# Performance work log

Measured on AMD Instinct MI355X. Metric: run time of the kernel, lower is better.

The kernel has to match this reference:

```python
import jax, jax.numpy as jnp
import numpy as np

NEG_SLOPE = 0.2
H = 2  # num_heads (hardcoded in the torch module)


def _gat_conv(x, W, al, ar, b, src, dst, n_nodes):
    """DGL GATConv: x [N,F] -> [N,H,D]."""
    D = al.shape[1]
    h = (x @ W).reshape(n_nodes, H, D)               # [N,H,D]
    el = jnp.einsum('nhd,hd->nh', h, al)              # [N,H]
    er = jnp.einsum('nhd,hd->nh', h, ar)              # [N,H]
    e = el[src] + er[dst]                             # [E,H]
    e = jnp.where(e >= 0, e, NEG_SLOPE * e)           # LeakyReLU
    # edge softmax over incoming edges of each dst (every node has a self loop)
    m = jax.ops.segment_max(e, dst, num_segments=n_nodes)      # [N,H]
    ex = jnp.exp(e - m[dst])                                    # [E,H]
    s = jax.ops.segment_sum(ex, dst, num_segments=n_nodes)     # [N,H]
    alpha = ex / s[dst]                                         # [E,H]
    msg = alpha[:, :, None] * h[src]                             # [E,H,D]
    out = jax.ops.segment_sum(msg, dst, num_segments=n_nodes)   # [N,H,D]
    return out + b.reshape(1, H, D)


def setup_inputs() -> dict:
    key = jax.random.key(0)
    ks = jax.random.split(key, 10)
    N, E, F_IN, HID, OUT = 100000, 1600000, 128, 64, 64
    sc = 0.05
    return {
        'x':   jax.random.normal(ks[0], (N, F_IN), jnp.float32),
        'src': jax.random.randint(ks[1], (E,), 0, N, jnp.int32),
        'dst': jax.random.randint(ks[2], (E,), 0, N, jnp.int32),
        'W1':  jax.random.normal(ks[3], (F_IN, H * HID), jnp.float32) * sc,
        'al1': jax.random.normal(ks[4], (H, HID), jnp.float32) * sc,
        'ar1': jax.random.normal(ks[5], (H, HID), jnp.float32) * sc,
        'b1':  jnp.zeros((H * HID,), jnp.float32),
        'W2':  jax.random.normal(ks[6], (H * HID, H * OUT), jnp.float32) * sc,
        'al2': jax.random.normal(ks[7], (H, OUT), jnp.float32) * sc,
        'ar2': jax.random.normal(ks[8], (H, OUT), jnp.float32) * sc,
        'b2':  jnp.zeros((H * OUT,), jnp.float32),
    }


def reference(x, src, dst, W1, al1, ar1, b1, W2, al2, ar2, b2):
    N = x.shape[0]
    # dgl.add_self_loop
    loop = jnp.arange(N, dtype=src.dtype)
    s = jnp.concatenate([src, loop])
    d = jnp.concatenate([dst, loop])
    h = _gat_conv(x, W1, al1, ar1, b1, s, d, N)       # [N,H,HID]
    h = jax.nn.relu(h).reshape(N, -1)                  # flatten heads
    out = _gat_conv(h, W2, al2, ar2, b2, s, d, N)      # [N,H,OUT]
    return out.reshape(N, -1)
```

## Files before the change

kernel.cpp:

```cpp
#include <hip/hip_runtime.h>
#include <hip/hip_fp16.h>


#define NEG_SLOPE 0.2f
#define BSHIFT 8
#define ETILE 4096

typedef _Float16 half8_t __attribute__((ext_vector_type(8)));
typedef float f32x4_t __attribute__((ext_vector_type(4)));


__global__ __launch_bounds__(256) void k_bcount(const int* __restrict__ dst, int E,
                                                int nbuck, int* __restrict__ bcnt) {
    __shared__ int cnt[512];
    int t = threadIdx.x;
    for (int b = t; b < nbuck; b += 256) cnt[b] = 0;
    __syncthreads();
    int e0 = blockIdx.x * ETILE;
    #pragma unroll
    for (int j = 0; j < ETILE / 256; j++) {
        int e = e0 + j * 256 + t;
        if (e < E) atomicAdd(&cnt[dst[e] >> BSHIFT], 1);
    }
    __syncthreads();
    for (int b = t; b < nbuck; b += 256) {
        int c = cnt[b];
        if (c > 0) atomicAdd(&bcnt[b], c);
    }
}

__global__ __launch_bounds__(256) void k_bscan(const int* __restrict__ bcnt, int nbuck,
                                               int* __restrict__ bbase,
                                               int* __restrict__ bcursor,
                                               int* __restrict__ rowStart, int N, int E) {
    __shared__ int sa[512], sb[512];
    int t = threadIdx.x;
    sa[t] = (t < nbuck) ? bcnt[t] : 0;
    sa[t + 256] = (t + 256 < nbuck) ? bcnt[t + 256] : 0;
    __syncthreads();
    int* a = sa;
    int* b = sb;
    for (int off = 1; off < 512; off <<= 1) {
        b[t] = a[t] + ((t >= off) ? a[t - off] : 0);
        int i = t + 256;
        b[i] = a[i] + ((i >= off) ? a[i - off] : 0);
        __syncthreads();
        int* tmp = a; a = b; b = tmp;
    }
    #pragma unroll
    for (int k = 0; k < 2; k++) {
        int i = t + k * 256;
        if (i <= nbuck) {
            int e_ = (i == 0) ? 0 : a[i - 1];
            bbase[i] = e_;
            if (i < nbuck) bcursor[i] = e_;
        }
    }
    if (t == 0) rowStart[N] = E;
}

__global__ __launch_bounds__(256) void k_bucket(const int* __restrict__ src,
                                                const int* __restrict__ dst, int E,
                                                int nbuck, int* __restrict__ bcursor,
                                                int* __restrict__ ebuf) {
    __shared__ int cnt[512];
    __shared__ int base[512];
    int t = threadIdx.x;
    for (int b = t; b < nbuck; b += 256) cnt[b] = 0;
    __syncthreads();
    int e0 = blockIdx.x * ETILE;
    int dv[ETILE / 256], sv[ETILE / 256];
    #pragma unroll
    for (int j = 0; j < ETILE / 256; j++) {
        int e = e0 + j * 256 + t;
        dv[j] = -1;
        if (e < E) {
            dv[j] = dst[e];
            sv[j] = src[e];
            atomicAdd(&cnt[dv[j] >> BSHIFT], 1);
        }
    }
    __syncthreads();
    for (int b = t; b < nbuck; b += 256) {
        int c = cnt[b];
        base[b] = (c > 0) ? atomicAdd(&bcursor[b], c) : 0;
    }
    __syncthreads();
    for (int b = t; b < nbuck; b += 256) cnt[b] = 0;
    __syncthreads();
    #pragma unroll
    for (int j = 0; j < ETILE / 256; j++) {
        if (dv[j] >= 0) {
            int bk = dv[j] >> BSHIFT;
            int r = atomicAdd(&cnt[bk], 1);
            ebuf[base[bk] + r] = sv[j] | ((dv[j] & ((1 << BSHIFT) - 1)) << 17);
        }
    }
}

__global__ __launch_bounds__(256) void k_build(const int* __restrict__ ebuf,
                                               const int* __restrict__ bbase,
                                               int* __restrict__ rowStart,
                                               int* __restrict__ csr, int N) {
    __shared__ int dcnt[256];
    __shared__ int sa[256], sb[256];
    __shared__ int cur[256];
    int b = blockIdx.x;
    int t = threadIdx.x;
    int lo = bbase[b], hi = bbase[b + 1];
    int n0 = b << BSHIFT;
    dcnt[t] = 0;
    __syncthreads();
    for (int p = lo + t; p < hi; p += 256)
        atomicAdd(&dcnt[((unsigned)ebuf[p]) >> 17], 1);
    __syncthreads();
    sa[t] = dcnt[t];
    __syncthreads();
    int* a = sa;
    int* bq = sb;
    for (int off = 1; off < 256; off <<= 1) {
        bq[t] = a[t] + ((t >= off) ? a[t - off] : 0);
        __syncthreads();
        int* tmp = a; a = bq; bq = tmp;
    }
    int excl = (t == 0) ? 0 : a[t - 1];
    int pos0 = lo + excl;
    if (n0 + t < N) rowStart[n0 + t] = pos0;
    cur[t] = pos0;
    __syncthreads();
    for (int p = lo + t; p < hi; p += 256) {
        int v = ebuf[p];
        int pos = atomicAdd(&cur[((unsigned)v) >> 17], 1);
        csr[pos] = v & 0x1FFFF;
    }
}


__global__ __launch_bounds__(256) void k_prep(const float* __restrict__ W1,
                                              const float* __restrict__ W2,
                                              __half* __restrict__ wh1,
                                              __half* __restrict__ wh2,
                                              int* __restrict__ bcnt, int nbuck) {
    int b = blockIdx.x;
    if (b >= 16) {
        for (int i = threadIdx.x; i < nbuck; i += 256) bcnt[i] = 0;
        return;
    }
    const float* W = (b < 8) ? W1 : W2;
    __half* Wh = (b < 8) ? wh1 : wh2;
    int q = (b & 7) * 256 + threadIdx.x;
    int r = q >> 4;
    int c = q & 15;
    int cl = c ^ (r & 7);
    float f[8];
    #pragma unroll
    for (int j = 0; j < 8; j++) f[j] = W[(size_t)(cl * 8 + j) * 128 + r];
    __half2 h0 = __floats2half2_rn(f[0], f[1]);
    __half2 h1 = __floats2half2_rn(f[2], f[3]);
    __half2 h2 = __floats2half2_rn(f[4], f[5]);
    __half2 h3 = __floats2half2_rn(f[6], f[7]);
    uint4 pk;
    pk.x = *(unsigned*)&h0;
    pk.y = *(unsigned*)&h1;
    pk.z = *(unsigned*)&h2;
    pk.w = *(unsigned*)&h3;
    *(uint4*)((char*)Wh + (size_t)q * 16) = pk;
}


__device__ __forceinline__ void g2l16(const void* g, void* l) {
    __builtin_amdgcn_global_load_lds((const __attribute__((address_space(1))) void*)g,
                                     (__attribute__((address_space(3))) void*)l, 16, 0, 0);
}

template <bool FP16IN>
__global__ __launch_bounds__(256, 3) void k_gemm_fused(const void* __restrict__ Ain,
                                                       const __half* __restrict__ WhT,
                                                       __half* __restrict__ hb,
                                                       const float* __restrict__ al,
                                                       const float* __restrict__ ar,
                                                       float* __restrict__ el,
                                                       float* __restrict__ er, int M) {
    __shared__ __half xs[64 * 128];
    __shared__ __half ws[128 * 128];
    int row0 = blockIdx.x * 64;
    int t = threadIdx.x;

    for (int j = 0; j < 8; j++) {
        int c16 = t + j * 256;
        g2l16((const char*)WhT + (size_t)c16 * 16, (char*)ws + (size_t)c16 * 16);
    }
    if (FP16IN) {
        const char* Ah = (const char*)Ain;
        for (int j = 0; j < 4; j++) {
            int c16 = t + j * 256;
            g2l16(Ah + (size_t)row0 * 256 + (size_t)c16 * 16, (char*)xs + (size_t)c16 * 16);
        }
    } else {
        const float* A = (const float*)Ain;
        for (int j = 0; j < 8; j++) {
            int f4 = t + j * 256;
            int r = f4 >> 5;
            int gr = row0 + r;
            if (gr >= M) gr = M - 1;
            float4 v = ((const float4*)(A + (size_t)gr * 128))[f4 & 31];
            __half2 h0 = __floats2half2_rn(v.x, v.y);
            __half2 h1 = __floats2half2_rn(v.z, v.w);
            uint2 pk;
            pk.x = *(unsigned*)&h0;
            pk.y = *(unsigned*)&h1;
            int h8 = f4 & 31;
            int c = h8 >> 1, hh = h8 & 1;
            int addr8 = r * 32 + (c ^ (r & 7)) * 2 + hh;
            *(uint2*)((char*)xs + (size_t)addr8 * 8) = pk;
        }
    }
    __syncthreads();

    int wid = t >> 6, lane = t & 63;
    int l15 = lane & 15;
    int g = lane >> 4;
    int mrow = wid * 16 + l15;

    half8_t xf[4];
    #pragma unroll
    for (int ks = 0; ks < 4; ks++) {
        int c = ks * 4 + g;
        xf[ks] = *(const half8_t*)((const char*)xs + mrow * 256 + (size_t)(c ^ (mrow & 7)) * 16);
    }

    f32x4_t acc[8];
    #pragma unroll
    for (int i = 0; i < 8; i++) acc[i] = (f32x4_t){0.f, 0.f, 0.f, 0.f};

    #pragma unroll
    for (int nt = 0; nt < 8; nt++) {
        int nrow = nt * 16 + l15;
        #pragma unroll
        for (int ks = 0; ks < 4; ks++) {
            int c = ks * 4 + g;
            half8_t wf = *(const half8_t*)((const char*)ws + nrow * 256 + (size_t)(c ^ (nrow & 7)) * 16);
            acc[nt] = __builtin_amdgcn_mfma_f32_16x16x32_f16(wf, xf[ks], acc[nt], 0, 0, 0);
        }
    }

    int m = row0 + wid * 16 + l15;
    bool valid = m < M;
    float plh0 = 0.f, prh0 = 0.f, plh1 = 0.f, prh1 = 0.f;
    #pragma unroll
    for (int nt = 0; nt < 8; nt++) {
        int col0 = nt * 16 + g * 4;
        if (valid) {
            __half2 p0 = __floats2half2_rn(acc[nt][0], acc[nt][1]);
            __half2 p1 = __floats2half2_rn(acc[nt][2], acc[nt][3]);
            uint2 pk;
            pk.x = *(unsigned*)&p0;
            pk.y = *(unsigned*)&p1;
            *(uint2*)(hb + (size_t)m * 128 + col0) = pk;
        }
        float4 alv = *(const float4*)(al + col0);
        float4 arv = *(const float4*)(ar + col0);
        float pl = acc[nt][0] * alv.x + acc[nt][1] * alv.y + acc[nt][2] * alv.z + acc[nt][3] * alv.w;
        float pr = acc[nt][0] * arv.x + acc[nt][1] * arv.y + acc[nt][2] * arv.z + acc[nt][3] * arv.w;
        if (nt < 4) { plh0 += pl; prh0 += pr; }
        else       { plh1 += pl; prh1 += pr; }
    }
    plh0 += __shfl_xor(plh0, 16); plh0 += __shfl_xor(plh0, 32);
    plh1 += __shfl_xor(plh1, 16); plh1 += __shfl_xor(plh1, 32);
    prh0 += __shfl_xor(prh0, 16); prh0 += __shfl_xor(prh0, 32);
    prh1 += __shfl_xor(prh1, 16); prh1 += __shfl_xor(prh1, 32);
    if (lane < 16 && valid) {
        el[m * 2 + 0] = plh0;
        el[m * 2 + 1] = plh1;
        er[m * 2 + 0] = prh0;
        er[m * 2 + 1] = prh1;
    }
}


__device__ __forceinline__ float h2f(__half h) { return __half2float(h); }

template <bool RELU, bool FP16OUT>
__global__ __launch_bounds__(256) void k_agg(const __half* __restrict__ hb,
                                             const float* __restrict__ el,
                                             const float* __restrict__ er,
                                             const int* __restrict__ rowStart,
                                             const int* __restrict__ csr,
                                             const float* __restrict__ bias,
                                             void* __restrict__ outv, int N) {
    __shared__ uint2 albuf[4][64];
    int wave = threadIdx.x >> 6;
    int lane = threadIdx.x & 63;
    int n = blockIdx.x * 4 + wave;
    if (n >= N) return;

    int rs = rowStart[n];
    int deg = rowStart[n + 1] - rs;
    float2 erv = ((const float2*)er)[n];

    if (deg < 64) {
        int sreg = n;
        float e0 = -3e38f, e1 = -3e38f;
        if (lane <= deg) {
            sreg = (lane == deg) ? n : csr[rs + lane];
            float2 ev = ((const float2*)el)[sreg];
            e0 = ev.x + erv.x;
            e0 = (e0 >= 0.f) ? e0 : NEG_SLOPE * e0;
            e1 = ev.y + erv.y;
            e1 = (e1 >= 0.f) ? e1 : NEG_SLOPE * e1;
        }
        float ex0 = __expf(e0);
        float ex1 = __expf(e1);
        float s0 = ex0, s1 = ex1;
        for (int off = 32; off > 0; off >>= 1) {
            s0 += __shfl_xor(s0, off);
            s1 += __shfl_xor(s1, off);
        }
        __half2 ah = __floats2half2_rn(ex0 * (1.0f / s0), ex1 * (1.0f / s1));
        uint2 pk;
        pk.x = (unsigned)sreg;
        pk.y = *(unsigned*)&ah;
        albuf[wave][lane] = pk;

        int q = lane >> 4;
        int c = lane & 15;
        float acc0 = 0.f, acc1 = 0.f, acc2 = 0.f, acc3 = 0.f;
        float acc4 = 0.f, acc5 = 0.f, acc6 = 0.f, acc7 = 0.f;
        int iters = (deg + 4) >> 2;
        #pragma unroll 4
        for (int kk = 0; kk < iters; ++kk) {
            int j = 4 * kk + q;
            uint2 pj = albuf[wave][j];
            __half2 ahj = *(__half2*)&pj.y;
            float a = (c >= 8) ? h2f(ahj.y) : h2f(ahj.x);
            uint4 hv = ((const uint4*)(hb + (size_t)pj.x * 128))[c];
            __half2 h0 = *(__half2*)&hv.x;
            __half2 h1 = *(__half2*)&hv.y;
            __half2 h2 = *(__half2*)&hv.z;
            __half2 h3 = *(__half2*)&hv.w;
            acc0 += a * h2f(h0.x);  acc1 += a * h2f(h0.y);
            acc2 += a * h2f(h1.x);  acc3 += a * h2f(h1.y);
            acc4 += a * h2f(h2.x);  acc5 += a * h2f(h2.y);
            acc6 += a * h2f(h3.x);  acc7 += a * h2f(h3.y);
        }
        acc0 += __shfl_xor(acc0, 16); acc1 += __shfl_xor(acc1, 16);
        acc2 += __shfl_xor(acc2, 16); acc3 += __shfl_xor(acc3, 16);
        acc4 += __shfl_xor(acc4, 16); acc5 += __shfl_xor(acc5, 16);
        acc6 += __shfl_xor(acc6, 16); acc7 += __shfl_xor(acc7, 16);
        acc0 += __shfl_xor(acc0, 32); acc1 += __shfl_xor(acc1, 32);
        acc2 += __shfl_xor(acc2, 32); acc3 += __shfl_xor(acc3, 32);
        acc4 += __shfl_xor(acc4, 32); acc5 += __shfl_xor(acc5, 32);
        acc6 += __shfl_xor(acc6, 32); acc7 += __shfl_xor(acc7, 32);
        if (lane < 16) {
            const float4* bp = (const float4*)(bias + c * 8);
            float4 b0 = bp[0], b1 = bp[1];
            float o0 = acc0 + b0.x, o1 = acc1 + b0.y, o2 = acc2 + b0.z, o3 = acc3 + b0.w;
            float o4 = acc4 + b1.x, o5 = acc5 + b1.y, o6 = acc6 + b1.z, o7 = acc7 + b1.w;
            if (RELU) {
                o0 = fmaxf(o0, 0.f); o1 = fmaxf(o1, 0.f); o2 = fmaxf(o2, 0.f); o3 = fmaxf(o3, 0.f);
                o4 = fmaxf(o4, 0.f); o5 = fmaxf(o5, 0.f); o6 = fmaxf(o6, 0.f); o7 = fmaxf(o7, 0.f);
            }
            if (FP16OUT) {
                __half2 q0 = __floats2half2_rn(o0, o1);
                __half2 q1 = __floats2half2_rn(o2, o3);
                __half2 q2 = __floats2half2_rn(o4, o5);
                __half2 q3 = __floats2half2_rn(o6, o7);
                uint4 opk;
                opk.x = *(unsigned*)&q0;
                opk.y = *(unsigned*)&q1;
                opk.z = *(unsigned*)&q2;
                opk.w = *(unsigned*)&q3;
                ((uint4*)((__half*)outv + (size_t)n * 128))[c ^ (n & 7)] = opk;
            } else {
                float* op = (float*)outv + (size_t)n * 128 + c * 8;
                ((float4*)op)[0] = make_float4(o0, o1, o2, o3);
                ((float4*)op)[1] = make_float4(o4, o5, o6, o7);
            }
        }
    } else {
        float m0 = -3e38f, m1 = -3e38f;
        for (int i = lane; i <= deg; i += 64) {
            int s = (i == deg) ? n : csr[rs + i];
            float2 ev = ((const float2*)el)[s];
            float e0 = ev.x + erv.x;
            e0 = (e0 >= 0.f) ? e0 : NEG_SLOPE * e0;
            float e1 = ev.y + erv.y;
            e1 = (e1 >= 0.f) ? e1 : NEG_SLOPE * e1;
            m0 = fmaxf(m0, e0);
            m1 = fmaxf(m1, e1);
        }
        for (int off = 32; off > 0; off >>= 1) {
            m0 = fmaxf(m0, __shfl_xor(m0, off));
            m1 = fmaxf(m1, __shfl_xor(m1, off));
        }
        float s0 = 0.f, s1 = 0.f;
        for (int i = lane; i <= deg; i += 64) {
            int s = (i == deg) ? n : csr[rs + i];
            float2 ev = ((const float2*)el)[s];
            float e0 = ev.x + erv.x;
            e0 = (e0 >= 0.f) ? e0 : NEG_SLOPE * e0;
            float e1 = ev.y + erv.y;
            e1 = (e1 >= 0.f) ? e1 : NEG_SLOPE * e1;
            s0 += __expf(e0 - m0);
            s1 += __expf(e1 - m1);
        }
        for (int off = 32; off > 0; off >>= 1) {
            s0 += __shfl_xor(s0, off);
            s1 += __shfl_xor(s1, off);
        }
        float inv0 = 1.0f / s0, inv1 = 1.0f / s1;
        float mh = (lane < 32) ? m0 : m1;
        float invh = (lane < 32) ? inv0 : inv1;
        float erh = (lane < 32) ? erv.x : erv.y;
        float a0 = 0.f, a1 = 0.f;
        for (int j = 0; j <= deg; j++) {
            int sj = (j == deg) ? n : csr[rs + j];
            float elh = el[sj * 2 + (lane >> 5)];
            float e = elh + erh;
            e = (e >= 0.f) ? e : NEG_SLOPE * e;
            float alpha = __expf(e - mh) * invh;
            unsigned hv = ((const unsigned*)(hb + (size_t)sj * 128))[lane];
            __half2 h = *(__half2*)&hv;
            a0 += alpha * h2f(h.x);
            a1 += alpha * h2f(h.y);
        }
        float2 bv = ((const float2*)bias)[lane];
        a0 += bv.x;
        a1 += bv.y;
        if (RELU) {
            a0 = fmaxf(a0, 0.f);
            a1 = fmaxf(a1, 0.f);
        }
        if (FP16OUT) {
            __half2 hv2 = __floats2half2_rn(a0, a1);
            int chunk = lane >> 2;
            int sub = lane & 3;
            *(unsigned*)((char*)outv + (size_t)n * 256 +
                         (size_t)((chunk ^ (n & 7)) * 16 + sub * 4)) = *(unsigned*)&hv2;
        } else {
            ((float2*)((float*)outv + (size_t)n * 128))[lane] = make_float2(a0, a1);
        }
    }
}


static inline size_t align_up(size_t v, size_t a) { return (v + a - 1) & ~(a - 1); }

extern "C" void kernel_launch(void* const* d_in, const int* in_sizes, int n_in,
                              void* d_out, int out_size, void* d_ws, size_t ws_size,
                              hipStream_t stream) {
    const float* x   = (const float*)d_in[0];
    const int*   src = (const int*)d_in[1];
    const int*   dst = (const int*)d_in[2];
    const float* W1  = (const float*)d_in[3];
    const float* al1 = (const float*)d_in[4];
    const float* ar1 = (const float*)d_in[5];
    const float* b1  = (const float*)d_in[6];
    const float* W2  = (const float*)d_in[7];
    const float* al2 = (const float*)d_in[8];
    const float* ar2 = (const float*)d_in[9];
    const float* b2  = (const float*)d_in[10];
    float* out = (float*)d_out;

    const int N = in_sizes[0] / 128;
    const int E = in_sizes[1];
    const int NBUCK = (N + 255) >> 8;

    char* ws = (char*)d_ws;
    size_t off = 0;
    __half* bufBh = (__half*)(ws + off); off = align_up(off + (size_t)N * 128 * 2, 256);
    __half* hb    = (__half*)(ws + off); off = align_up(off + (size_t)N * 128 * 2, 256);
    float* el   = (float*)(ws + off); off = align_up(off + (size_t)N * 2 * 4, 256);
    float* er   = (float*)(ws + off); off = align_up(off + (size_t)N * 2 * 4, 256);
    int* rowStart = (int*)(ws + off); off = align_up(off + (size_t)(N + 1) * 4, 256);
    int* csr      = (int*)(ws + off); off = align_up(off + (size_t)E * 4, 256);
    int* ebuf     = (int*)(ws + off); off = align_up(off + (size_t)E * 4, 256);
    int* bcnt     = (int*)(ws + off); off = align_up(off + (size_t)NBUCK * 4, 256);
    int* bbase    = (int*)(ws + off); off = align_up(off + (size_t)(NBUCK + 1) * 4, 256);
    int* bcursor  = (int*)(ws + off); off = align_up(off + (size_t)NBUCK * 4, 256);
    __half* wh1   = (__half*)(ws + off); off = align_up(off + (size_t)16384 * 2, 256);
    __half* wh2   = (__half*)(ws + off); off = align_up(off + (size_t)16384 * 2, 256);

    const int etile_grid = (E + ETILE - 1) / ETILE;

    k_prep<<<17, 256, 0, stream>>>(W1, W2, wh1, wh2, bcnt, NBUCK);
    k_bcount<<<etile_grid, 256, 0, stream>>>(dst, E, NBUCK, bcnt);
    k_bscan<<<1, 256, 0, stream>>>(bcnt, NBUCK, bbase, bcursor, rowStart, N, E);
    k_bucket<<<etile_grid, 256, 0, stream>>>(src, dst, E, NBUCK, bcursor, ebuf);
    k_build<<<NBUCK, 256, 0, stream>>>(ebuf, bbase, rowStart, csr, N);

    const int gemm_grid = (N + 63) / 64;
    const int agg_grid = (N + 3) / 4;

    k_gemm_fused<false><<<gemm_grid, 256, 0, stream>>>(x, wh1, hb, al1, ar1, el, er, N);
    k_agg<true, true><<<agg_grid, 256, 0, stream>>>(hb, el, er, rowStart, csr, b1, bufBh, N);

    k_gemm_fused<true><<<gemm_grid, 256, 0, stream>>>(bufBh, wh2, hb, al2, ar2, el, er, N);
    k_agg<false, false><<<agg_grid, 256, 0, stream>>>(hb, el, er, rowStart, csr, b2, out, N);
}
```

Before: 236.6 us.

## Split aggregation into alpha pass and column-sliced gather over sliced feature layout

The GEMM now writes node features in eight 16-column slices, each a contiguous 32-byte-per-node array. A new k_alpha kernel computes the per-edge softmax weights and stores packed (src, alpha) records. A new k_aggs kernel gathers one slice per block so each slice's working set fits in cache. The intent is better L2 locality for the random gather, at the cost of an extra kernel, an extra E-sized record buffer write and read, and eight passes over the edge records.

Measured after the change: 628.8 us. 2.66x slower.

```diff
diff --git a/kernel.cpp b/kernel.cpp
--- a/kernel.cpp
+++ b/kernel.cpp
@@ -5,9 +5,11 @@
 #define NEG_SLOPE 0.2f
 #define BSHIFT 8
 #define ETILE 4096
+#define NPW 8
 
 typedef _Float16 half8_t __attribute__((ext_vector_type(8)));
 typedef float f32x4_t __attribute__((ext_vector_type(4)));
+typedef unsigned long long u64;
 
 
 __global__ __launch_bounds__(256) void k_bcount(const int* __restrict__ dst, int E,
@@ -176,7 +178,7 @@
 template <bool FP16IN>
 __global__ __launch_bounds__(256, 3) void k_gemm_fused(const void* __restrict__ Ain,
                                                        const __half* __restrict__ WhT,
-                                                       __half* __restrict__ hb,
+                                                       __half* __restrict__ hbs,
                                                        const float* __restrict__ al,
                                                        const float* __restrict__ ar,
                                                        float* __restrict__ el,
@@ -253,10 +255,9 @@
         if (valid) {
             __half2 p0 = __floats2half2_rn(acc[nt][0], acc[nt][1]);
             __half2 p1 = __floats2half2_rn(acc[nt][2], acc[nt][3]);
-            uint2 pk;
-            pk.x = *(unsigned*)&p0;
-            pk.y = *(unsigned*)&p1;
-            *(uint2*)(hb + (size_t)m * 128 + col0) = pk;
+            u64 w = ((u64)(*(unsigned*)&p1) << 32) | (u64)(*(unsigned*)&p0);
+            __builtin_nontemporal_store(
+                w, (u64*)((char*)hbs + ((size_t)nt * M + m) * 32 + (size_t)g * 8));
         }
         float4 alv = *(const float4*)(al + col0);
         float4 arv = *(const float4*)(ar + col0);
@@ -280,30 +281,26 @@
 
 __device__ __forceinline__ float h2f(__half h) { return __half2float(h); }
 
-template <bool RELU, bool FP16OUT>
-__global__ __launch_bounds__(256) void k_agg(const __half* __restrict__ hb,
-                                             const float* __restrict__ el,
-                                             const float* __restrict__ er,
-                                             const int* __restrict__ rowStart,
-                                             const int* __restrict__ csr,
-                                             const float* __restrict__ bias,
-                                             void* __restrict__ outv, int N) {
-    __shared__ uint2 albuf[4][64];
+__global__ __launch_bounds__(256) void k_alpha(const float* __restrict__ el,
+                                               const float* __restrict__ er,
+                                               const int* __restrict__ rowStart,
+                                               const int* __restrict__ csr,
+                                               u64* __restrict__ ea, int N) {
     int wave = threadIdx.x >> 6;
     int lane = threadIdx.x & 63;
     int n = blockIdx.x * 4 + wave;
     if (n >= N) return;
-
     int rs = rowStart[n];
     int deg = rowStart[n + 1] - rs;
     float2 erv = ((const float2*)er)[n];
+    size_t base = (size_t)rs + n;
 
     if (deg < 64) {
-        int sreg = n;
+        int sj = n;
         float e0 = -3e38f, e1 = -3e38f;
         if (lane <= deg) {
-            sreg = (lane == deg) ? n : csr[rs + lane];
-            float2 ev = ((const float2*)el)[sreg];
+            sj = (lane == deg) ? n : csr[rs + lane];
+            float2 ev = ((const float2*)el)[sj];
             e0 = ev.x + erv.x;
             e0 = (e0 >= 0.f) ? e0 : NEG_SLOPE * e0;
             e1 = ev.y + erv.y;
@@ -316,66 +313,10 @@
             s0 += __shfl_xor(s0, off);
             s1 += __shfl_xor(s1, off);
         }
-        __half2 ah = __floats2half2_rn(ex0 * (1.0f / s0), ex1 * (1.0f / s1));
-        uint2 pk;
-        pk.x = (unsigned)sreg;
-        pk.y = *(unsigned*)&ah;
-        albuf[wave][lane] = pk;
-
-        int q = lane >> 4;
-        int c = lane & 15;
-        float acc0 = 0.f, acc1 = 0.f, acc2 = 0.f, acc3 = 0.f;
-        float acc4 = 0.f, acc5 = 0.f, acc6 = 0.f, acc7 = 0.f;
-        int iters = (deg + 4) >> 2;
-        #pragma unroll 4
-        for (int kk = 0; kk < iters; ++kk) {
-            int j = 4 * kk + q;
-            uint2 pj = albuf[wave][j];
-            __half2 ahj = *(__half2*)&pj.y;
-            float a = (c >= 8) ? h2f(ahj.y) : h2f(ahj.x);
-            uint4 hv = ((const uint4*)(hb + (size_t)pj.x * 128))[c];
-            __half2 h0 = *(__half2*)&hv.x;
-            __half2 h1 = *(__half2*)&hv.y;
-            __half2 h2 = *(__half2*)&hv.z;
-            __half2 h3 = *(__half2*)&hv.w;
-            acc0 += a * h2f(h0.x);  acc1 += a * h2f(h0.y);
-            acc2 += a * h2f(h1.x);  acc3 += a * h2f(h1.y);
-            acc4 += a * h2f(h2.x);  acc5 += a * h2f(h2.y);
-            acc6 += a * h2f(h3.x);  acc7 += a * h2f(h3.y);
-        }
-        acc0 += __shfl_xor(acc0, 16); acc1 += __shfl_xor(acc1, 16);
-        acc2 += __shfl_xor(acc2, 16); acc3 += __shfl_xor(acc3, 16);
-        acc4 += __shfl_xor(acc4, 16); acc5 += __shfl_xor(acc5, 16);
-        acc6 += __shfl_xor(acc6, 16); acc7 += __shfl_xor(acc7, 16);
-        acc0 += __shfl_xor(acc0, 32); acc1 += __shfl_xor(acc1, 32);
-        acc2 += __shfl_xor(acc2, 32); acc3 += __shfl_xor(acc3, 32);
-        acc4 += __shfl_xor(acc4, 32); acc5 += __shfl_xor(acc5, 32);
-        acc6 += __shfl_xor(acc6, 32); acc7 += __shfl_xor(acc7, 32);
-        if (lane < 16) {
-            const float4* bp = (const float4*)(bias + c * 8);
-            float4 b0 = bp[0], b1 = bp[1];
-            float o0 = acc0 + b0.x, o1 = acc1 + b0.y, o2 = acc2 + b0.z, o3 = acc3 + b0.w;
-            float o4 = acc4 + b1.x, o5 = acc5 + b1.y, o6 = acc6 + b1.z, o7 = acc7 + b1.w;
-            if (RELU) {
-                o0 = fmaxf(o0, 0.f); o1 = fmaxf(o1, 0.f); o2 = fmaxf(o2, 0.f); o3 = fmaxf(o3, 0.f);
-                o4 = fmaxf(o4, 0.f); o5 = fmaxf(o5, 0.f); o6 = fmaxf(o6, 0.f); o7 = fmaxf(o7, 0.f);
-            }
-            if (FP16OUT) {
-                __half2 q0 = __floats2half2_rn(o0, o1);
-                __half2 q1 = __floats2half2_rn(o2, o3);
-                __half2 q2 = __floats2half2_rn(o4, o5);
-                __half2 q3 = __floats2half2_rn(o6, o7);
-                uint4 opk;
-                opk.x = *(unsigned*)&q0;
-                opk.y = *(unsigned*)&q1;
-                opk.z = *(unsigned*)&q2;
-                opk.w = *(unsigned*)&q3;
-                ((uint4*)((__half*)outv + (size_t)n * 128))[c ^ (n & 7)] = opk;
-            } else {
-                float* op = (float*)outv + (size_t)n * 128 + c * 8;
-                ((float4*)op)[0] = make_float4(o0, o1, o2, o3);
-                ((float4*)op)[1] = make_float4(o4, o5, o6, o7);
-            }
+        if (lane <= deg) {
+            __half2 ah = __floats2half2_rn(ex0 * (1.0f / s0), ex1 * (1.0f / s1));
+            u64 rec = ((u64)(*(unsigned*)&ah) << 32) | (u64)(unsigned)sj;
+            __builtin_nontemporal_store(rec, ea + base + lane);
         }
     } else {
         float m0 = -3e38f, m1 = -3e38f;
@@ -409,36 +350,89 @@
             s1 += __shfl_xor(s1, off);
         }
         float inv0 = 1.0f / s0, inv1 = 1.0f / s1;
-        float mh = (lane < 32) ? m0 : m1;
-        float invh = (lane < 32) ? inv0 : inv1;
-        float erh = (lane < 32) ? erv.x : erv.y;
-        float a0 = 0.f, a1 = 0.f;
-        for (int j = 0; j <= deg; j++) {
-            int sj = (j == deg) ? n : csr[rs + j];
-            float elh = el[sj * 2 + (lane >> 5)];
-            float e = elh + erh;
-            e = (e >= 0.f) ? e : NEG_SLOPE * e;
-            float alpha = __expf(e - mh) * invh;
-            unsigned hv = ((const unsigned*)(hb + (size_t)sj * 128))[lane];
-            __half2 h = *(__half2*)&hv;
-            a0 += alpha * h2f(h.x);
-            a1 += alpha * h2f(h.y);
-        }
-        float2 bv = ((const float2*)bias)[lane];
-        a0 += bv.x;
-        a1 += bv.y;
-        if (RELU) {
-            a0 = fmaxf(a0, 0.f);
-            a1 = fmaxf(a1, 0.f);
-        }
-        if (FP16OUT) {
-            __half2 hv2 = __floats2half2_rn(a0, a1);
-            int chunk = lane >> 2;
-            int sub = lane & 3;
-            *(unsigned*)((char*)outv + (size_t)n * 256 +
-                         (size_t)((chunk ^ (n & 7)) * 16 + sub * 4)) = *(unsigned*)&hv2;
-        } else {
-            ((float2*)((float*)outv + (size_t)n * 128))[lane] = make_float2(a0, a1);
+        for (int i = lane; i <= deg; i += 64) {
+            int s = (i == deg) ? n : csr[rs + i];
+            float2 ev = ((const float2*)el)[s];
+            float e0 = ev.x + erv.x;
+            e0 = (e0 >= 0.f) ? e0 : NEG_SLOPE * e0;
+            float e1 = ev.y + erv.y;
+            e1 = (e1 >= 0.f) ? e1 : NEG_SLOPE * e1;
+            __half2 ah = __floats2half2_rn(__expf(e0 - m0) * inv0, __expf(e1 - m1) * inv1);
+            u64 rec = ((u64)(*(unsigned*)&ah) << 32) | (u64)(unsigned)s;
+            __builtin_nontemporal_store(rec, ea + base + i);
+        }
+    }
+}
+
+
+template <bool RELU, bool FP16OUT>
+__global__ __launch_bounds__(256) void k_aggs(const u64* __restrict__ ea,
+                                              const __half* __restrict__ hbs,
+                                              const int* __restrict__ rowStart,
+                                              const float* __restrict__ bias,
+                                              void* __restrict__ outv, int N) {
+    int s = blockIdx.x & 7;
+    int ng = blockIdx.x >> 3;
+    int wid = threadIdx.x >> 6;
+    int lane = threadIdx.x & 63;
+    int g = lane >> 2;
+    int d = lane & 3;
+    const char* slice = (const char*)hbs + (size_t)s * N * 32;
+    float4 bv = *(const float4*)(bias + s * 16 + d * 4);
+    bool head1 = (s >= 4);
+    int n0 = (ng * 4 + wid) * NPW;
+
+    for (int ni = 0; ni < NPW; ni++) {
+        int n = n0 + ni;
+        if (n >= N) return;
+        int rs = rowStart[n];
+        int cnt = rowStart[n + 1] - rs + 1;
+        size_t base = (size_t)rs + n;
+        float a0 = 0.f, a1 = 0.f, a2 = 0.f, a3 = 0.f;
+        for (int j0 = 0; j0 < cnt; j0 += 16) {
+            int j = j0 + g;
+            if (j < cnt) {
+                u64 rec = __builtin_nontemporal_load(ea + base + j);
+                unsigned srcn = (unsigned)rec;
+                unsigned ab = (unsigned)(rec >> 32);
+                unsigned short hbits = (unsigned short)(head1 ? (ab >> 16) : (ab & 0xffff));
+                __half ha;
+                *(unsigned short*)&ha = hbits;
+                float a = h2f(ha);
+                uint2 hv = *(const uint2*)(slice + (size_t)srcn * 32 + (size_t)d * 8);
+                __half2 p0 = *(__half2*)&hv.x;
+                __half2 p1 = *(__half2*)&hv.y;
+                a0 += a * h2f(p0.x);
+                a1 += a * h2f(p0.y);
+                a2 += a * h2f(p1.x);
+                a3 += a * h2f(p1.y);
+            }
+        }
+        #pragma unroll
+        for (int off = 4; off < 64; off <<= 1) {
+            a0 += __shfl_xor(a0, off);
+            a1 += __shfl_xor(a1, off);
+            a2 += __shfl_xor(a2, off);
+            a3 += __shfl_xor(a3, off);
+        }
+        if (g == 0) {
+            a0 += bv.x; a1 += bv.y; a2 += bv.z; a3 += bv.w;
+            if (RELU) {
+                a0 = fmaxf(a0, 0.f); a1 = fmaxf(a1, 0.f);
+                a2 = fmaxf(a2, 0.f); a3 = fmaxf(a3, 0.f);
+            }
+            if (FP16OUT) {
+                __half2 q0 = __floats2half2_rn(a0, a1);
+                __half2 q1 = __floats2half2_rn(a2, a3);
+                u64 w = ((u64)(*(unsigned*)&q1) << 32) | (u64)(*(unsigned*)&q0);
+                int c = 2 * s + (d >> 1);
+                size_t addr = (size_t)n * 256 + (size_t)((c ^ (n & 7)) * 16 + (d & 1) * 8);
+                __builtin_nontemporal_store(w, (u64*)((char*)outv + addr));
+            } else {
+                f32x4_t o = {a0, a1, a2, a3};
+                __builtin_nontemporal_store(
+                    o, (f32x4_t*)((float*)outv + (size_t)n * 128 + s * 16 + d * 4));
+            }
         }
     }
 }
@@ -469,12 +463,13 @@
     char* ws = (char*)d_ws;
     size_t off = 0;
     __half* bufBh = (__half*)(ws + off); off = align_up(off + (size_t)N * 128 * 2, 256);
-    __half* hb    = (__half*)(ws + off); off = align_up(off + (size_t)N * 128 * 2, 256);
+    __half* hbs   = (__half*)(ws + off); off = align_up(off + (size_t)N * 128 * 2, 256);
     float* el   = (float*)(ws + off); off = align_up(off + (size_t)N * 2 * 4, 256);
     float* er   = (float*)(ws + off); off = align_up(off + (size_t)N * 2 * 4, 256);
     int* rowStart = (int*)(ws + off); off = align_up(off + (size_t)(N + 1) * 4, 256);
     int* csr      = (int*)(ws + off); off = align_up(off + (size_t)E * 4, 256);
     int* ebuf     = (int*)(ws + off); off = align_up(off + (size_t)E * 4, 256);
+    u64* ea       = (u64*)(ws + off); off = align_up(off + (size_t)(E + N) * 8, 256);
     int* bcnt     = (int*)(ws + off); off = align_up(off + (size_t)NBUCK * 4, 256);
     int* bbase    = (int*)(ws + off); off = align_up(off + (size_t)(NBUCK + 1) * 4, 256);
     int* bcursor  = (int*)(ws + off); off = align_up(off + (size_t)NBUCK * 4, 256);
@@ -490,11 +485,14 @@
     k_build<<<NBUCK, 256, 0, stream>>>(ebuf, bbase, rowStart, csr, N);
 
     const int gemm_grid = (N + 63) / 64;
-    const int agg_grid = (N + 3) / 4;
-
-    k_gemm_fused<false><<<gemm_grid, 256, 0, stream>>>(x, wh1, hb, al1, ar1, el, er, N);
-    k_agg<true, true><<<agg_grid, 256, 0, stream>>>(hb, el, er, rowStart, csr, b1, bufBh, N);
-
-    k_gemm_fused<true><<<gemm_grid, 256, 0, stream>>>(bufBh, wh2, hb, al2, ar2, el, er, N);
-    k_agg<false, false><<<agg_grid, 256, 0, stream>>>(hb, el, er, rowStart, csr, b2, out, N);
-}
+    const int alpha_grid = (N + 3) / 4;
+    const int aggs_grid = 8 * ((N + 4 * NPW - 1) / (4 * NPW));
+
+    k_gemm_fused<false><<<gemm_grid, 256, 0, stream>>>(x, wh1, hbs, al1, ar1, el, er, N);
+    k_alpha<<<alpha_grid, 256, 0, stream>>>(el, er, rowStart, csr, ea, N);
+    k_aggs<true, true><<<aggs_grid, 256, 0, stream>>>(ea, hbs, rowStart, b1, bufBh, N);
+
+    k_gemm_fused<true><<<gemm_grid, 256, 0, stream>>>(bufBh, wh2, hbs, al2, ar2, el, er, N);
+    k_alpha<<<alpha_grid, 256, 0, stream>>>(el, er, rowStart, csr, ea, N);
+    k_aggs<false, false><<<aggs_grid, 256, 0, stream>>>(ea, hbs, rowStart, b2, out, N);
+}
```

## Pack four nodes per wave in aggregation and fuse bucket count into GEMM

Applied to the files above, without the earlier changes.

The aggregation kernel now assigns a 16-lane quarter-wave to each destination node instead of a full wave. It computes unnormalized exponentials in one pass without a max subtraction and applies the softmax normalization once at the end. This is meant to remove wasted lanes on low-degree nodes and the separate max pass. The dst bucket-count kernel is folded into the first GEMM launch as extra blocks, saving one launch. Dropping the max subtraction risks overflow if attention logits grow large.

Measured after the change: 228.2 us. 3.6% less time.

```diff
diff --git a/kernel.cpp b/kernel.cpp
--- a/kernel.cpp
+++ b/kernel.cpp
@@ -8,26 +8,8 @@
 
 typedef _Float16 half8_t __attribute__((ext_vector_type(8)));
 typedef float f32x4_t __attribute__((ext_vector_type(4)));
-
-
-__global__ __launch_bounds__(256) void k_bcount(const int* __restrict__ dst, int E,
-                                                int nbuck, int* __restrict__ bcnt) {
-    __shared__ int cnt[512];
-    int t = threadIdx.x;
-    for (int b = t; b < nbuck; b += 256) cnt[b] = 0;
-    __syncthreads();
-    int e0 = blockIdx.x * ETILE;
-    #pragma unroll
-    for (int j = 0; j < ETILE / 256; j++) {
-        int e = e0 + j * 256 + t;
-        if (e < E) atomicAdd(&cnt[dst[e] >> BSHIFT], 1);
-    }
-    __syncthreads();
-    for (int b = t; b < nbuck; b += 256) {
-        int c = cnt[b];
-        if (c > 0) atomicAdd(&bcnt[b], c);
-    }
-}
+typedef unsigned long long u64;
+
 
 __global__ __launch_bounds__(256) void k_bscan(const int* __restrict__ bcnt, int nbuck,
                                                int* __restrict__ bbase,
@@ -173,19 +155,40 @@
                                      (__attribute__((address_space(3))) void*)l, 16, 0, 0);
 }
 
-template <bool FP16IN>
+template <bool FP16IN, bool COUNT>
 __global__ __launch_bounds__(256, 3) void k_gemm_fused(const void* __restrict__ Ain,
                                                        const __half* __restrict__ WhT,
                                                        __half* __restrict__ hb,
                                                        const float* __restrict__ al,
                                                        const float* __restrict__ ar,
                                                        float* __restrict__ el,
-                                                       float* __restrict__ er, int M) {
+                                                       float* __restrict__ er, int M,
+                                                       const int* __restrict__ dstE, int E,
+                                                       int nbuck, int* __restrict__ bcnt,
+                                                       int gemmBlocks) {
     __shared__ __half xs[64 * 128];
     __shared__ __half ws[128 * 128];
+    int t = threadIdx.x;
+
+    if (COUNT && (int)blockIdx.x >= gemmBlocks) {
+        int* cnt = (int*)xs;
+        for (int b = t; b < nbuck; b += 256) cnt[b] = 0;
+        __syncthreads();
+        int e0 = ((int)blockIdx.x - gemmBlocks) * ETILE;
+        #pragma unroll
+        for (int j = 0; j < ETILE / 256; j++) {
+            int e = e0 + j * 256 + t;
+            if (e < E) atomicAdd(&cnt[dstE[e] >> BSHIFT], 1);
+        }
+        __syncthreads();
+        for (int b = t; b < nbuck; b += 256) {
+            int c = cnt[b];
+            if (c > 0) atomicAdd(&bcnt[b], c);
+        }
+        return;
+    }
+
     int row0 = blockIdx.x * 64;
-    int t = threadIdx.x;
-
     for (int j = 0; j < 8; j++) {
         int c16 = t + j * 256;
         g2l16((const char*)WhT + (size_t)c16 * 16, (char*)ws + (size_t)c16 * 16);
@@ -288,157 +291,114 @@
                                              const int* __restrict__ csr,
                                              const float* __restrict__ bias,
                                              void* __restrict__ outv, int N) {
-    __shared__ uint2 albuf[4][64];
-    int wave = threadIdx.x >> 6;
+    __shared__ u64 albuf[4][4][65];
+    int wid = threadIdx.x >> 6;
     int lane = threadIdx.x & 63;
-    int n = blockIdx.x * 4 + wave;
-    if (n >= N) return;
-
-    int rs = rowStart[n];
-    int deg = rowStart[n + 1] - rs;
-    float2 erv = ((const float2*)er)[n];
-
-    if (deg < 64) {
-        int sreg = n;
-        float e0 = -3e38f, e1 = -3e38f;
-        if (lane <= deg) {
-            sreg = (lane == deg) ? n : csr[rs + lane];
-            float2 ev = ((const float2*)el)[sreg];
-            e0 = ev.x + erv.x;
-            e0 = (e0 >= 0.f) ? e0 : NEG_SLOPE * e0;
-            e1 = ev.y + erv.y;
-            e1 = (e1 >= 0.f) ? e1 : NEG_SLOPE * e1;
-        }
-        float ex0 = __expf(e0);
-        float ex1 = __expf(e1);
-        float s0 = ex0, s1 = ex1;
-        for (int off = 32; off > 0; off >>= 1) {
-            s0 += __shfl_xor(s0, off);
-            s1 += __shfl_xor(s1, off);
-        }
-        __half2 ah = __floats2half2_rn(ex0 * (1.0f / s0), ex1 * (1.0f / s1));
-        uint2 pk;
-        pk.x = (unsigned)sreg;
-        pk.y = *(unsigned*)&ah;
-        albuf[wave][lane] = pk;
-
-        int q = lane >> 4;
-        int c = lane & 15;
-        float acc0 = 0.f, acc1 = 0.f, acc2 = 0.f, acc3 = 0.f;
-        float acc4 = 0.f, acc5 = 0.f, acc6 = 0.f, acc7 = 0.f;
-        int iters = (deg + 4) >> 2;
-        #pragma unroll 4
-        for (int kk = 0; kk < iters; ++kk) {
-            int j = 4 * kk + q;
-            uint2 pj = albuf[wave][j];
-            __half2 ahj = *(__half2*)&pj.y;
-            float a = (c >= 8) ? h2f(ahj.y) : h2f(ahj.x);
-            uint4 hv = ((const uint4*)(hb + (size_t)pj.x * 128))[c];
-            __half2 h0 = *(__half2*)&hv.x;
-            __half2 h1 = *(__half2*)&hv.y;
-            __half2 h2 = *(__half2*)&hv.z;
-            __half2 h3 = *(__half2*)&hv.w;
-            acc0 += a * h2f(h0.x);  acc1 += a * h2f(h0.y);
-            acc2 += a * h2f(h1.x);  acc3 += a * h2f(h1.y);
-            acc4 += a * h2f(h2.x);  acc5 += a * h2f(h2.y);
-            acc6 += a * h2f(h3.x);  acc7 += a * h2f(h3.y);
-        }
-        acc0 += __shfl_xor(acc0, 16); acc1 += __shfl_xor(acc1, 16);
-        acc2 += __shfl_xor(acc2, 16); acc3 += __shfl_xor(acc3, 16);
-        acc4 += __shfl_xor(acc4, 16); acc5 += __shfl_xor(acc5, 16);
-        acc6 += __shfl_xor(acc6, 16); acc7 += __shfl_xor(acc7, 16);
-        acc0 += __shfl_xor(acc0, 32); acc1 += __shfl_xor(acc1, 32);
-        acc2 += __shfl_xor(acc2, 32); acc3 += __shfl_xor(acc3, 32);
-        acc4 += __shfl_xor(acc4, 32); acc5 += __shfl_xor(acc5, 32);
-        acc6 += __shfl_xor(acc6, 32); acc7 += __shfl_xor(acc7, 32);
-        if (lane < 16) {
-            const float4* bp = (const float4*)(bias + c * 8);
-            float4 b0 = bp[0], b1 = bp[1];
-            float o0 = acc0 + b0.x, o1 = acc1 + b0.y, o2 = acc2 + b0.z, o3 = acc3 + b0.w;
-            float o4 = acc4 + b1.x, o5 = acc5 + b1.y, o6 = acc6 + b1.z, o7 = acc7 + b1.w;
-            if (RELU) {
-                o0 = fmaxf(o0, 0.f); o1 = fmaxf(o1, 0.f); o2 = fmaxf(o2, 0.f); o3 = fmaxf(o3, 0.f);
-                o4 = fmaxf(o4, 0.f); o5 = fmaxf(o5, 0.f); o6 = fmaxf(o6, 0.f); o7 = fmaxf(o7, 0.f);
-            }
-            if (FP16OUT) {
-                __half2 q0 = __floats2half2_rn(o0, o1);
-                __half2 q1 = __floats2half2_rn(o2, o3);
-                __half2 q2 = __floats2half2_rn(o4, o5);
-                __half2 q3 = __floats2half2_rn(o6, o7);
-                uint4 opk;
-                opk.x = *(unsigned*)&q0;
-                opk.y = *(unsigned*)&q1;
-                opk.z = *(unsigned*)&q2;
-                opk.w = *(unsigned*)&q3;
-                ((uint4*)((__half*)outv + (size_t)n * 128))[c ^ (n & 7)] = opk;
-            } else {
-                float* op = (float*)outv + (size_t)n * 128 + c * 8;
-                ((float4*)op)[0] = make_float4(o0, o1, o2, o3);
-                ((float4*)op)[1] = make_float4(o4, o5, o6, o7);
-            }
-        }
-    } else {
-        float m0 = -3e38f, m1 = -3e38f;
-        for (int i = lane; i <= deg; i += 64) {
+    int q = lane >> 4;
+    int l = lane & 15;
+    int n = (blockIdx.x * 4 + wid) * 4 + q;
+    bool active = n < N;
+
+    int rs = 0, deg = 0;
+    float2 erv = make_float2(0.f, 0.f);
+    if (active) {
+        rs = rowStart[n];
+        deg = rowStart[n + 1] - rs;
+        erv = ((const float2*)er)[n];
+    }
+
+    float s0 = 0.f, s1 = 0.f;
+    if (active) {
+        for (int i = l; i <= deg; i += 16) {
             int s = (i == deg) ? n : csr[rs + i];
             float2 ev = ((const float2*)el)[s];
             float e0 = ev.x + erv.x;
             e0 = (e0 >= 0.f) ? e0 : NEG_SLOPE * e0;
             float e1 = ev.y + erv.y;
             e1 = (e1 >= 0.f) ? e1 : NEG_SLOPE * e1;
-            m0 = fmaxf(m0, e0);
-            m1 = fmaxf(m1, e1);
-        }
-        for (int off = 32; off > 0; off >>= 1) {
-            m0 = fmaxf(m0, __shfl_xor(m0, off));
-            m1 = fmaxf(m1, __shfl_xor(m1, off));
-        }
-        float s0 = 0.f, s1 = 0.f;
-        for (int i = lane; i <= deg; i += 64) {
-            int s = (i == deg) ? n : csr[rs + i];
+            float ex0 = __expf(e0);
+            float ex1 = __expf(e1);
+            s0 += ex0;
+            s1 += ex1;
+            if (i < 64) {
+                __half2 eh = __floats2half2_rn(ex0, ex1);
+                albuf[wid][q][i] = ((u64)(*(unsigned*)&eh) << 32) | (u64)(unsigned)s;
+            }
+        }
+    }
+    #pragma unroll
+    for (int mk = 8; mk >= 1; mk >>= 1) {
+        s0 += __shfl_xor(s0, mk);
+        s1 += __shfl_xor(s1, mk);
+    }
+    bool hi = l >= 8;
+    float invh = hi ? (1.0f / s1) : (1.0f / s0);
+
+    float a0 = 0.f, a1 = 0.f, a2 = 0.f, a3 = 0.f;
+    float a4 = 0.f, a5 = 0.f, a6 = 0.f, a7 = 0.f;
+    if (active) {
+        int cnt = deg + 1;
+        int jmax = (cnt < 64) ? cnt : 64;
+        #pragma unroll 4
+        for (int j = 0; j < jmax; ++j) {
+            u64 rec = albuf[wid][q][j];
+            unsigned srcn = (unsigned)rec;
+            unsigned eb = (unsigned)(rec >> 32);
+            __half hx;
+            *(unsigned short*)&hx = (unsigned short)(hi ? (eb >> 16) : (eb & 0xffff));
+            float a = h2f(hx);
+            uint4 hv = ((const uint4*)(hb + (size_t)srcn * 128))[l];
+            __half2 p0 = *(__half2*)&hv.x;
+            __half2 p1 = *(__half2*)&hv.y;
+            __half2 p2 = *(__half2*)&hv.z;
+            __half2 p3 = *(__half2*)&hv.w;
+            a0 += a * h2f(p0.x);  a1 += a * h2f(p0.y);
+            a2 += a * h2f(p1.x);  a3 += a * h2f(p1.y);
+            a4 += a * h2f(p2.x);  a5 += a * h2f(p2.y);
+            a6 += a * h2f(p3.x);  a7 += a * h2f(p3.y);
+        }
+        for (int j = 64; j < cnt; ++j) {
+            int s = (j == deg) ? n : csr[rs + j];
             float2 ev = ((const float2*)el)[s];
-            float e0 = ev.x + erv.x;
-            e0 = (e0 >= 0.f) ? e0 : NEG_SLOPE * e0;
-            float e1 = ev.y + erv.y;
-            e1 = (e1 >= 0.f) ? e1 : NEG_SLOPE * e1;
-            s0 += __expf(e0 - m0);
-            s1 += __expf(e1 - m1);
-        }
-        for (int off = 32; off > 0; off >>= 1) {
-            s0 += __shfl_xor(s0, off);
-            s1 += __shfl_xor(s1, off);
-        }
-        float inv0 = 1.0f / s0, inv1 = 1.0f / s1;
-        float mh = (lane < 32) ? m0 : m1;
-        float invh = (lane < 32) ? inv0 : inv1;
-        float erh = (lane < 32) ? erv.x : erv.y;
-        float a0 = 0.f, a1 = 0.f;
-        for (int j = 0; j <= deg; j++) {
-            int sj = (j == deg) ? n : csr[rs + j];
-            float elh = el[sj * 2 + (lane >> 5)];
-            float e = elh + erh;
+            float e = hi ? (ev.y + erv.y) : (ev.x + erv.x);
             e = (e >= 0.f) ? e : NEG_SLOPE * e;
-            float alpha = __expf(e - mh) * invh;
-            unsigned hv = ((const unsigned*)(hb + (size_t)sj * 128))[lane];
-            __half2 h = *(__half2*)&hv;
-            a0 += alpha * h2f(h.x);
-            a1 += alpha * h2f(h.y);
-        }
-        float2 bv = ((const float2*)bias)[lane];
-        a0 += bv.x;
-        a1 += bv.y;
+            float a = __expf(e);
+            uint4 hv = ((const uint4*)(hb + (size_t)s * 128))[l];
+            __half2 p0 = *(__half2*)&hv.x;
+            __half2 p1 = *(__half2*)&hv.y;
+            __half2 p2 = *(__half2*)&hv.z;
+            __half2 p3 = *(__half2*)&hv.w;
+            a0 += a * h2f(p0.x);  a1 += a * h2f(p0.y);
+            a2 += a * h2f(p1.x);  a3 += a * h2f(p1.y);
+            a4 += a * h2f(p2.x);  a5 += a * h2f(p2.y);
+            a6 += a * h2f(p3.x);  a7 += a * h2f(p3.y);
+        }
+
+        const float4* bp = (const float4*)(bias + l * 8);
+        float4 b0 = bp[0], b1 = bp[1];
+        a0 = a0 * invh + b0.x;  a1 = a1 * invh + b0.y;
+        a2 = a2 * invh + b0.z;  a3 = a3 * invh + b0.w;
+        a4 = a4 * invh + b1.x;  a5 = a5 * invh + b1.y;
+        a6 = a6 * invh + b1.z;  a7 = a7 * invh + b1.w;
         if (RELU) {
-            a0 = fmaxf(a0, 0.f);
-            a1 = fmaxf(a1, 0.f);
+            a0 = fmaxf(a0, 0.f); a1 = fmaxf(a1, 0.f); a2 = fmaxf(a2, 0.f); a3 = fmaxf(a3, 0.f);
+            a4 = fmaxf(a4, 0.f); a5 = fmaxf(a5, 0.f); a6 = fmaxf(a6, 0.f); a7 = fmaxf(a7, 0.f);
         }
         if (FP16OUT) {
-            __half2 hv2 = __floats2half2_rn(a0, a1);
-            int chunk = lane >> 2;
-            int sub = lane & 3;
-            *(unsigned*)((char*)outv + (size_t)n * 256 +
-                         (size_t)((chunk ^ (n & 7)) * 16 + sub * 4)) = *(unsigned*)&hv2;
+            __half2 q0 = __floats2half2_rn(a0, a1);
+            __half2 q1 = __floats2half2_rn(a2, a3);
+            __half2 q2 = __floats2half2_rn(a4, a5);
+            __half2 q3 = __floats2half2_rn(a6, a7);
+            uint4 opk;
+            opk.x = *(unsigned*)&q0;
+            opk.y = *(unsigned*)&q1;
+            opk.z = *(unsigned*)&q2;
+            opk.w = *(unsigned*)&q3;
+            ((uint4*)((__half*)outv + (size_t)n * 128))[l ^ (n & 7)] = opk;
         } else {
-            ((float2*)((float*)outv + (size_t)n * 128))[lane] = make_float2(a0, a1);
+            float* op = (float*)outv + (size_t)n * 128 + l * 8;
+            ((float4*)op)[0] = make_float4(a0, a1, a2, a3);
+            ((float4*)op)[1] = make_float4(a4, a5, a6, a7);
         }
     }
 }
@@ -469,7 +429,7 @@
     char* ws = (char*)d_ws;
     size_t off = 0;
     __half* bufBh = (__half*)(ws + off); off = align_up(off + (size_t)N * 128 * 2, 256);
-    __half* hb    = (__half*)(ws + off); off = align_up(off + (size_t)N * 128 * 2, 256);
+    __half* hb    = (__half*)(ws + off); off = align_up(off + (size_t)N * 128 * 2 + 16384, 256);
     float* el   = (float*)(ws + off); off = align_up(off + (size_t)N * 2 * 4, 256);
     float* er   = (float*)(ws + off); off = align_up(off + (size_t)N * 2 * 4, 256);
     int* rowStart = (int*)(ws + off); off = align_up(off + (size_t)(N + 1) * 4, 256);
@@ -482,19 +442,22 @@
     __half* wh2   = (__half*)(ws + off); off = align_up(off + (size_t)16384 * 2, 256);
 
     const int etile_grid = (E + ETILE - 1) / ETILE;
+    const int gemm_grid = (N + 63) / 64;
+    const int agg_grid = (N + 15) / 16;
 
     k_prep<<<17, 256, 0, stream>>>(W1, W2, wh1, wh2, bcnt, NBUCK);
-    k_bcount<<<etile_grid, 256, 0, stream>>>(dst, E, NBUCK, bcnt);
+
+    k_gemm_fused<false, true><<<gemm_grid + etile_grid, 256, 0, stream>>>(
+        x, wh1, hb, al1, ar1, el, er, N, dst, E, NBUCK, bcnt, gemm_grid);
+
     k_bscan<<<1, 256, 0, stream>>>(bcnt, NBUCK, bbase, bcursor, rowStart, N, E);
     k_bucket<<<etile_grid, 256, 0, stream>>>(src, dst, E, NBUCK, bcursor, ebuf);
     k_build<<<NBUCK, 256, 0, stream>>>(ebuf, bbase, rowStart, csr, N);
 
-    const int gemm_grid = (N + 63) / 64;
-    const int agg_grid = (N + 3) / 4;
-
-    k_gemm_fused<false><<<gemm_grid, 256, 0, stream>>>(x, wh1, hb, al1, ar1, el, er, N);
     k_agg<true, true><<<agg_grid, 256, 0, stream>>>(hb, el, er, rowStart, csr, b1, bufBh, N);
 
-    k_gemm_fused<true><<<gemm_grid, 256, 0, stream>>>(bufBh, wh2, hb, al2, ar2, el, er, N);
+    k_gemm_fused<true, false><<<gemm_grid, 256, 0, stream>>>(
+        bufBh, wh2, hb, al2, ar2, el, er, N, nullptr, 0, 0, nullptr, gemm_grid);
+
     k_agg<false, false><<<agg_grid, 256, 0, stream>>>(hb, el, er, rowStart, csr, b2, out, N);
 }
```
